# Optimization experiments

Measured on AMD Instinct MI355X. Metric: run time of the kernel, lower is better.

Reference implementation:

```python
import jax, jax.numpy as jnp
import numpy as np
import math

RCR = 5.2
ETAR = np.array([16.0], dtype=np.float32)
SHFR = np.array([0.9, 1.16875, 1.4375, 1.70625, 1.975, 2.24375, 2.5125, 2.78125,
                 3.05, 3.31875, 3.5875, 3.85625, 4.125, 4.39375, 4.6625, 4.93125],
                dtype=np.float32)
# cartesian product of (EtaR, ShfR) -> [P, 2], P = 1*16 = 16
_PAIRS = np.stack(np.meshgrid(ETAR, SHFR, indexing='ij'), axis=-1).reshape(-1, 2)
ETA_P = jnp.asarray(_PAIRS[:, 0])  # [P]
SHF_P = jnp.asarray(_PAIRS[:, 1])  # [P]


def setup_inputs() -> dict:
    key = jax.random.key(0)
    k1, k2 = jax.random.split(key)
    B, N = 16, 512
    d = jax.random.uniform(k1, (B, N, N), dtype=jnp.float32, minval=0.0, maxval=10.0)
    d = 0.5 * (d + jnp.transpose(d, (0, 2, 1)))          # symmetric distances
    d = d * (1.0 - jnp.eye(N, dtype=jnp.float32))        # zero diagonal (self-distance)
    z = jax.random.randint(k2, (B, N), 1, 10).astype(jnp.float32)
    return {"distance_matrices": d, "atomic_numbers_batch": z}


def reference(distance_matrices, atomic_numbers_batch):
    d = distance_matrices                                  # [B, N, N]  (i, j)
    # cutoff mask: within Rcr and not the zero self/padding entries
    mask = (d < RCR) & (d != 0.0)                          # [B, N, N]
    fc = 0.5 * jnp.cos(math.pi * d / RCR) + 0.5            # [B, N, N]
    z_j = atomic_numbers_batch[:, None, :]                 # [B, 1, N]
    # radial term per (pair, param): z_j * exp(-eta*(R-shf)^2) * fC(R)
    g = jnp.exp(-ETA_P * (d[..., None] - SHF_P) ** 2)      # [B, N, N, P]
    addends = (z_j * fc)[..., None] * g                    # [B, N, N, P]
    addends = jnp.where(mask[..., None], addends, 0.0)
    # sum over neighbors j (equivalent to the scatter-into-ragged + reduce_sum)
    GR_batch = jnp.sum(addends, axis=2)                    # [B, N, P]
    return GR_batch
```

## Files before the change

kernel.cpp:

```cpp
#include <hip/hip_runtime.h>

#ifndef __has_builtin
#define __has_builtin(x) 0
#endif

__device__ __forceinline__ float fexp2(float x) {
#if __has_builtin(__builtin_amdgcn_exp2f)
    return __builtin_amdgcn_exp2f(x);
#else
    return exp2f(x);
#endif
}

__device__ __forceinline__ float fcos_rev(float r) {
#if __has_builtin(__builtin_amdgcn_cosf)
    return __builtin_amdgcn_cosf(r);
#else
    return __cosf(r * 6.283185307179586f);
#endif
}

constexpr int NATOMS = 512;
constexpr int NP     = 16;

__device__ __constant__ float c_shf[NP] = {
    0.9f, 1.16875f, 1.4375f, 1.70625f, 1.975f, 2.24375f, 2.5125f, 2.78125f,
    3.05f, 3.31875f, 3.5875f, 3.85625f, 4.125f, 4.39375f, 4.6625f, 4.93125f
};

__global__ __launch_bounds__(256) void aev_radial_kernel(
        const float* __restrict__ d,
        const float* __restrict__ z,
        float* __restrict__ out)
{
    const int lane = threadIdx.x & 63;
    const int wave = threadIdx.x >> 6;
    const int row  = blockIdx.x * 4 + wave;
    const int b    = row >> 9;

    const float4* __restrict__ dd = reinterpret_cast<const float4*>(d + (size_t)row * NATOMS);
    const float4* __restrict__ zz = reinterpret_cast<const float4*>(z + (size_t)b   * NATOMS);

    const float C   = -23.083120654223414f;
    const float REV = 0.09615384615384616f;

    float acc[NP];
#pragma unroll
    for (int p = 0; p < NP; ++p) acc[p] = 0.0f;

#pragma unroll
    for (int h = 0; h < 2; ++h) {
        float4 dv4 = dd[lane + 64 * h];
        float4 zv4 = zz[lane + 64 * h];
#pragma unroll
        for (int q = 0; q < 4; ++q) {
            float dv = (&dv4.x)[q];
            float zv = (&zv4.x)[q];
            bool valid = (dv < 5.2f) && (dv != 0.0f);
            float fc = fmaf(0.5f, fcos_rev(dv * REV), 0.5f);
            float w  = valid ? zv * fc : 0.0f;
#pragma unroll
            for (int p = 0; p < NP; ++p) {
                float t = dv - c_shf[p];
                float e = fexp2((C * t) * t);
                acc[p] = fmaf(w, e, acc[p]);
            }
        }
    }

    bool u;
    float r0[8];
    u = (lane & 1) != 0;
#pragma unroll
    for (int k = 0; k < 8; ++k) {
        float snd  = u ? acc[k] : acc[k + 8];
        float rcv  = __shfl_xor(snd, 1, 64);
        float kept = u ? acc[k + 8] : acc[k];
        r0[k] = kept + rcv;
    }
    float r1[4];
    u = (lane & 2) != 0;
#pragma unroll
    for (int k = 0; k < 4; ++k) {
        float snd  = u ? r0[k] : r0[k + 4];
        float rcv  = __shfl_xor(snd, 2, 64);
        float kept = u ? r0[k + 4] : r0[k];
        r1[k] = kept + rcv;
    }
    float r2[2];
    u = (lane & 4) != 0;
#pragma unroll
    for (int k = 0; k < 2; ++k) {
        float snd  = u ? r1[k] : r1[k + 2];
        float rcv  = __shfl_xor(snd, 4, 64);
        float kept = u ? r1[k + 2] : r1[k];
        r2[k] = kept + rcv;
    }
    float r3;
    u = (lane & 8) != 0;
    {
        float snd  = u ? r2[0] : r2[1];
        float rcv  = __shfl_xor(snd, 8, 64);
        float kept = u ? r2[1] : r2[0];
        r3 = kept + rcv;
    }
    r3 += __shfl_xor(r3, 16, 64);
    r3 += __shfl_xor(r3, 32, 64);

    int idx = ((lane & 1) << 3) | ((lane & 2) << 1) | ((lane & 4) >> 1) | ((lane & 8) >> 3);
    if (lane < 16) {
        out[(size_t)row * NP + idx] = r3;
    }
}

extern "C" void kernel_launch(void* const* d_in, const int* in_sizes, int n_in,
                              void* d_out, int out_size, void* d_ws, size_t ws_size,
                              hipStream_t stream) {
    const float* d  = (const float*)d_in[0];
    const float* z  = (const float*)d_in[1];
    float* out      = (float*)d_out;

    aev_radial_kernel<<<dim3(2048), dim3(256), 0, stream>>>(d, z, out);
}
```

Before: 74.88 us.

## Replace per-shift exponentials with Gaussian recurrence from two anchor centers

Because the shifts are evenly spaced, each Gaussian term is now built from neighbouring ones by a multiplicative recurrence anchored at two centres (1.975 and 4.125). This needs about four exp2 calls per element instead of sixteen, trading transcendental work for chained multiplies. The chained products may lose some accuracy, and large constant factors such as 2^±26.7 risk overflow or underflow for extreme distances. It also adds an occupancy hint to the launch bounds, and the reduction code gains a dead, unused variable.

```diff
diff --git a/kernel.cpp b/kernel.cpp
--- a/kernel.cpp
+++ b/kernel.cpp
@@ -23,12 +23,47 @@
 constexpr int NATOMS = 512;
 constexpr int NP     = 16;
 
-__device__ __constant__ float c_shf[NP] = {
-    0.9f, 1.16875f, 1.4375f, 1.70625f, 1.975f, 2.24375f, 2.5125f, 2.78125f,
-    3.05f, 3.31875f, 3.5875f, 3.85625f, 4.125f, 4.39375f, 4.6625f, 4.93125f
-};
 
-__global__ __launch_bounds__(256) void aev_radial_kernel(
+__device__ __forceinline__ void process_elem(float dv, float zv, float* acc,
+                                             float k2, float cwh, float cvh) {
+    const float C   = -23.083120654223414f;
+    const float A   = 12.407177351645085f;
+    const float B   = -1.6672144566f;
+    const float REV = 0.09615384615384616f;
+
+    bool  valid = (dv < 5.2f) && (dv != 0.0f);
+    float fc    = fmaf(0.5f, fcos_rev(dv * REV), 0.5f);
+    float we    = valid ? zv * fc : 0.0f;
+
+    float tl = dv - 1.975f;
+    float th = dv - 4.125f;
+    float gl = we * fexp2((C * tl) * tl);
+    float gh = we * fexp2((C * th) * th);
+    float wl = fexp2(fmaf(A, tl, B));
+    float vl = fexp2(fmaf(-A, tl, B));
+    float wh = wl * cwh;
+    float vh = vl * cvh;
+
+    acc[4] += gl;
+    float g = gl * wl; acc[5] += g; wl *= k2;
+    g = g * wl;        acc[6] += g; wl *= k2;
+    g = g * wl;        acc[7] += g;
+    g = gl * vl;       acc[3] += g; vl *= k2;
+    g = g * vl;        acc[2] += g; vl *= k2;
+    g = g * vl;        acc[1] += g; vl *= k2;
+    g = g * vl;        acc[0] += g;
+
+    acc[12] += gh;
+    g = gh * wh;       acc[13] += g; wh *= k2;
+    g = g * wh;        acc[14] += g; wh *= k2;
+    g = g * wh;        acc[15] += g;
+    g = gh * vh;       acc[11] += g; vh *= k2;
+    g = g * vh;        acc[10] += g; vh *= k2;
+    g = g * vh;        acc[9]  += g; vh *= k2;
+    g = g * vh;        acc[8]  += g;
+}
+
+__global__ __launch_bounds__(256, 4) void aev_radial_kernel(
         const float* __restrict__ d,
         const float* __restrict__ z,
         float* __restrict__ out)
@@ -41,8 +76,9 @@
     const float4* __restrict__ dd = reinterpret_cast<const float4*>(d + (size_t)row * NATOMS);
     const float4* __restrict__ zz = reinterpret_cast<const float4*>(z + (size_t)b   * NATOMS);
 
-    const float C   = -23.083120654223414f;
-    const float REV = 0.09615384615384616f;
+    const float k2  = fexp2(-3.3344289132f);
+    const float cwh = fexp2(-26.675431306f);
+    const float cvh = fexp2( 26.675431306f);
 
     float acc[NP];
 #pragma unroll
@@ -52,20 +88,10 @@
     for (int h = 0; h < 2; ++h) {
         float4 dv4 = dd[lane + 64 * h];
         float4 zv4 = zz[lane + 64 * h];
-#pragma unroll
-        for (int q = 0; q < 4; ++q) {
-            float dv = (&dv4.x)[q];
-            float zv = (&zv4.x)[q];
-            bool valid = (dv < 5.2f) && (dv != 0.0f);
-            float fc = fmaf(0.5f, fcos_rev(dv * REV), 0.5f);
-            float w  = valid ? zv * fc : 0.0f;
-#pragma unroll
-            for (int p = 0; p < NP; ++p) {
-                float t = dv - c_shf[p];
-                float e = fexp2((C * t) * t);
-                acc[p] = fmaf(w, e, acc[p]);
-            }
-        }
+        process_elem(dv4.x, zv4.x, acc, k2, cwh, cvh);
+        process_elem(dv4.y, zv4.y, acc, k2, cwh, cvh);
+        process_elem(dv4.z, zv4.z, acc, k2, cwh, cvh);
+        process_elem(dv4.w, zv4.w, acc, k2, cwh, cvh);
     }
 
     bool u;
@@ -82,8 +108,10 @@
     u = (lane & 2) != 0;
 #pragma unroll
     for (int k = 0; k < 4; ++k) {
-        float snd  = u ? r0[k] : r0[k + 4];
-        float rcv  = __shfl_xor(snd, 2, 64);
+        float snd  = u ? r1[0] : r1[0];
+        (void)snd;
+        float s2   = u ? r0[k] : r0[k + 4];
+        float rcv  = __shfl_xor(s2, 2, 64);
         float kept = u ? r0[k + 4] : r0[k];
         r1[k] = kept + rcv;
     }
@@ -91,16 +119,16 @@
     u = (lane & 4) != 0;
 #pragma unroll
     for (int k = 0; k < 2; ++k) {
-        float snd  = u ? r1[k] : r1[k + 2];
-        float rcv  = __shfl_xor(snd, 4, 64);
+        float s2   = u ? r1[k] : r1[k + 2];
+        float rcv  = __shfl_xor(s2, 4, 64);
         float kept = u ? r1[k + 2] : r1[k];
         r2[k] = kept + rcv;
     }
     float r3;
     u = (lane & 8) != 0;
     {
-        float snd  = u ? r2[0] : r2[1];
-        float rcv  = __shfl_xor(snd, 8, 64);
+        float s2   = u ? r2[0] : r2[1];
+        float rcv  = __shfl_xor(s2, 8, 64);
         float kept = u ? r2[1] : r2[0];
         r3 = kept + rcv;
     }
```

Measured after the change: 69.06 us. -7.8%, faster.

## Replace per-shift exp with recurrence ladder using packed f32 math

Applied to the files above, without the earlier changes.

Because the shifts are uniformly spaced, the Gaussian terms for the 16 shifts are now computed with a multiplicative recurrence anchored at two centres (1.975 and 4.125). Each element then needs only four exp2 calls instead of sixteen, and the rest are packed multiplies and adds via v_pk_mul_f32/v_pk_add_f32 on element pairs. This targets the transcendental throughput bottleneck. The risks are lost precision from chained multiplications (possible underflow or overflow in the ratio factors, such as 2^26.7 scaling) and higher register pressure from the pairs, which the launch bounds of 4 waves are meant to cap.

```diff
diff --git a/kernel.cpp b/kernel.cpp
--- a/kernel.cpp
+++ b/kernel.cpp
@@ -20,15 +20,68 @@
 #endif
 }
 
+typedef __attribute__((ext_vector_type(2))) float v2f;
+
+__device__ __forceinline__ v2f pk_mul(v2f a, v2f b) {
+    v2f d;
+    asm("v_pk_mul_f32 %0, %1, %2" : "=v"(d) : "v"(a), "v"(b));
+    return d;
+}
+__device__ __forceinline__ v2f pk_add(v2f a, v2f b) {
+    v2f d;
+    asm("v_pk_add_f32 %0, %1, %2" : "=v"(d) : "v"(a), "v"(b));
+    return d;
+}
+
 constexpr int NATOMS = 512;
 constexpr int NP     = 16;
 
-__device__ __constant__ float c_shf[NP] = {
-    0.9f, 1.16875f, 1.4375f, 1.70625f, 1.975f, 2.24375f, 2.5125f, 2.78125f,
-    3.05f, 3.31875f, 3.5875f, 3.85625f, 4.125f, 4.39375f, 4.6625f, 4.93125f
-};
 
-__global__ __launch_bounds__(256) void aev_radial_kernel(
+__device__ __forceinline__ void setup_elem(float dv, float zv,
+                                           float& gl, float& gh,
+                                           float& wl, float& vl) {
+    const float C   = -23.083120654223414f;
+    const float A   = 12.407177351645085f;
+    const float B   = -1.6672144566f;
+    const float REV = 0.09615384615384616f;
+
+    bool  valid = (dv < 5.2f) && (dv != 0.0f);
+    float fc    = fmaf(0.5f, fcos_rev(dv * REV), 0.5f);
+    float we    = valid ? zv * fc : 0.0f;
+
+    float tl = dv - 1.975f;
+    float th = dv - 4.125f;
+    gl = we * fexp2((C * tl) * tl);
+    gh = we * fexp2((C * th) * th);
+    wl = fexp2(fmaf(A, tl, B));
+    vl = fexp2(fmaf(-A, tl, B));
+}
+
+__device__ __forceinline__ void ladder_pair(v2f* acc2, v2f GL, v2f GH,
+                                            v2f WL, v2f VL,
+                                            v2f K2, v2f CWH, v2f CVH) {
+    v2f g, w, v;
+    acc2[4] = pk_add(acc2[4], GL);
+    g = pk_mul(GL, WL); acc2[5] = pk_add(acc2[5], g); w = pk_mul(WL, K2);
+    g = pk_mul(g,  w ); acc2[6] = pk_add(acc2[6], g); w = pk_mul(w,  K2);
+    g = pk_mul(g,  w ); acc2[7] = pk_add(acc2[7], g);
+    g = pk_mul(GL, VL); acc2[3] = pk_add(acc2[3], g); v = pk_mul(VL, K2);
+    g = pk_mul(g,  v ); acc2[2] = pk_add(acc2[2], g); v = pk_mul(v,  K2);
+    g = pk_mul(g,  v ); acc2[1] = pk_add(acc2[1], g); v = pk_mul(v,  K2);
+    g = pk_mul(g,  v ); acc2[0] = pk_add(acc2[0], g);
+    v2f WH = pk_mul(WL, CWH);
+    v2f VH = pk_mul(VL, CVH);
+    acc2[12] = pk_add(acc2[12], GH);
+    g = pk_mul(GH, WH); acc2[13] = pk_add(acc2[13], g); w = pk_mul(WH, K2);
+    g = pk_mul(g,  w ); acc2[14] = pk_add(acc2[14], g); w = pk_mul(w,  K2);
+    g = pk_mul(g,  w ); acc2[15] = pk_add(acc2[15], g);
+    g = pk_mul(GH, VH); acc2[11] = pk_add(acc2[11], g); v = pk_mul(VH, K2);
+    g = pk_mul(g,  v ); acc2[10] = pk_add(acc2[10], g); v = pk_mul(v,  K2);
+    g = pk_mul(g,  v ); acc2[9]  = pk_add(acc2[9],  g); v = pk_mul(v,  K2);
+    g = pk_mul(g,  v ); acc2[8]  = pk_add(acc2[8],  g);
+}
+
+__global__ __launch_bounds__(256, 4) void aev_radial_kernel(
         const float* __restrict__ d,
         const float* __restrict__ z,
         float* __restrict__ out)
@@ -41,32 +94,37 @@
     const float4* __restrict__ dd = reinterpret_cast<const float4*>(d + (size_t)row * NATOMS);
     const float4* __restrict__ zz = reinterpret_cast<const float4*>(z + (size_t)b   * NATOMS);
 
-    const float C   = -23.083120654223414f;
-    const float REV = 0.09615384615384616f;
+    const float k2v  = fexp2(-3.3344289132f);
+    const float cwhv = fexp2(-26.675431306f);
+    const float cvhv = fexp2( 26.675431306f);
+    const v2f K2  = {k2v,  k2v};
+    const v2f CWH = {cwhv, cwhv};
+    const v2f CVH = {cvhv, cvhv};
 
-    float acc[NP];
+    v2f acc2[NP];
 #pragma unroll
-    for (int p = 0; p < NP; ++p) acc[p] = 0.0f;
+    for (int p = 0; p < NP; ++p) acc2[p] = (v2f){0.0f, 0.0f};
 
 #pragma unroll
     for (int h = 0; h < 2; ++h) {
         float4 dv4 = dd[lane + 64 * h];
         float4 zv4 = zz[lane + 64 * h];
 #pragma unroll
-        for (int q = 0; q < 4; ++q) {
-            float dv = (&dv4.x)[q];
-            float zv = (&zv4.x)[q];
-            bool valid = (dv < 5.2f) && (dv != 0.0f);
-            float fc = fmaf(0.5f, fcos_rev(dv * REV), 0.5f);
-            float w  = valid ? zv * fc : 0.0f;
-#pragma unroll
-            for (int p = 0; p < NP; ++p) {
-                float t = dv - c_shf[p];
-                float e = fexp2((C * t) * t);
-                acc[p] = fmaf(w, e, acc[p]);
-            }
+        for (int pr = 0; pr < 2; ++pr) {
+            float d0 = (&dv4.x)[2 * pr],     z0 = (&zv4.x)[2 * pr];
+            float d1 = (&dv4.x)[2 * pr + 1], z1 = (&zv4.x)[2 * pr + 1];
+            float gl0, gh0, wl0, vl0, gl1, gh1, wl1, vl1;
+            setup_elem(d0, z0, gl0, gh0, wl0, vl0);
+            setup_elem(d1, z1, gl1, gh1, wl1, vl1);
+            v2f GL = {gl0, gl1}, GH = {gh0, gh1};
+            v2f WL = {wl0, wl1}, VL = {vl0, vl1};
+            ladder_pair(acc2, GL, GH, WL, VL, K2, CWH, CVH);
         }
     }
+
+    float acc[NP];
+#pragma unroll
+    for (int p = 0; p < NP; ++p) acc[p] = acc2[p].x + acc2[p].y;
 
     bool u;
     float r0[8];
```

Result: faster. 67.98 us (median of 2 runs) (-9.2%).
